# Kernel optimization log

Measured on AMD Instinct MI355X. Metric: run time of the kernel, lower is better.

The kernel has to match this reference:

```python
import jax, jax.numpy as jnp
import numpy as np

B, CH, T = 8, 512, 1024
HEADS = 8
KC = CH // HEADS  # 64
BLOCK = 256       # block_length


def setup_inputs() -> dict:
    key = jax.random.key(0)
    ks = jax.random.split(key, 10)
    s = 0.05
    x = jax.random.normal(ks[0], (B, CH, T), jnp.float32)
    c = jax.random.normal(ks[1], (B, CH, T), jnp.float32)
    attn_mask = jnp.ones((1, 1, T, T), jnp.int32)
    # 1x1 Conv1d weights are just [out, in] matrices over the channel dim.
    Wq = jax.random.normal(ks[2], (CH, CH), jnp.float32) * s
    bq = jax.random.normal(ks[3], (CH,), jnp.float32) * s
    Wk = jax.random.normal(ks[4], (CH, CH), jnp.float32) * s
    bk = jax.random.normal(ks[5], (CH,), jnp.float32) * s
    Wv = jax.random.normal(ks[6], (CH, CH), jnp.float32) * s
    bv = jax.random.normal(ks[7], (CH,), jnp.float32) * s
    Wo = jax.random.normal(ks[8], (CH, CH), jnp.float32) * s
    bo = jax.random.normal(ks[9], (CH,), jnp.float32) * s
    return {"x": x, "c": c, "attn_mask": attn_mask,
            "Wq": Wq, "bq": bq, "Wk": Wk, "bk": bk,
            "Wv": Wv, "bv": bv, "Wo": Wo, "bo": bo}


def _proj(W, b, z):
    # 1x1 Conv1d: [B,C,T] -> [B,O,T]
    return jnp.einsum('oc,bct->bot', W, z) + b[None, :, None]


def reference(x, c, attn_mask, Wq, bq, Wk, bk, Wv, bv, Wo, bo):
    q = _proj(Wq, bq, x)
    k = _proj(Wk, bk, c)
    v = _proj(Wv, bv, c)

    def split_heads(z):  # [B,C,T] -> [B,H,T,KC]
        return z.reshape(B, HEADS, KC, T).transpose(0, 1, 3, 2)

    qh, kh, vh = split_heads(q), split_heads(k), split_heads(v)

    scale = jnp.asarray(1.0 / np.sqrt(KC), qh.dtype)
    scores = jnp.einsum('bhtd,bhsd->bhts', qh * scale, kh)  # [B,H,T,T]

    r = jnp.arange(T)
    diff = jnp.abs(r[None, :] - r[:, None])  # |i - j|, [T,T]
    # proximal bias: -log(1 + |i-j|)
    scores = scores + (-jnp.log1p(diff.astype(scores.dtype)))[None, None]
    # attention mask: masked_fill(mask == 0, -1e4)
    scores = jnp.where(attn_mask == 0, jnp.asarray(-1e4, scores.dtype), scores)
    # block-length band mask: keep |i-j| <= BLOCK (triu(-BLOCK).tril(BLOCK))
    band = (diff <= BLOCK)[None, None]
    scores = jnp.where(band, scores, jnp.asarray(-1e4, scores.dtype))

    p_attn = jax.nn.softmax(scores, axis=-1)
    out = jnp.einsum('bhts,bhsd->bhtd', p_attn, vh)  # [B,H,T,KC]
    out = out.transpose(0, 1, 3, 2).reshape(B, CH, T)  # merge heads -> [B,C,T]
    return _proj(Wo, bo, out)
```

## Files before the change

kernel.cpp:

```cpp
#include <hip/hip_runtime.h>
#include <stdint.h>

typedef unsigned short u16;
typedef __attribute__((ext_vector_type(8))) __bf16 bf16x8;
typedef __attribute__((ext_vector_type(4))) float f32x4;

constexpr int B_ = 8, CH = 512, T = 1024, NH = 8, HD = 64, BAND = 256;

__device__ inline u16 f2b(float f) {
  union { float f; uint32_t u; } v; v.f = f;
  uint32_t r = (v.u + 0x7fffu + ((v.u >> 16) & 1u)) >> 16;
  return (u16)r;
}

__device__ inline f32x4 mfma16(bf16x8 a, bf16x8 b, f32x4 c) {
  return __builtin_amdgcn_mfma_f32_16x16x32_bf16(a, b, c, 0, 0, 0);
}

__device__ __forceinline__ void gld16(const void* g, void* l) {
  __builtin_amdgcn_global_load_lds((__attribute__((address_space(1))) void*)(g),
                                   (__attribute__((address_space(3))) void*)(l),
                                   16, 0, 0);
}

__device__ __forceinline__ float exp2_hw(float x) { return __builtin_amdgcn_exp2f(x); }

__global__ __launch_bounds__(256) void cvt_w(const float* __restrict__ wq, const float* __restrict__ wk,
                                             const float* __restrict__ wv, const float* __restrict__ wo,
                                             u16* __restrict__ out) {
  int idx = blockIdx.x * 256 + threadIdx.x;
  int w = idx >> 15;
  const float* src = (w == 0) ? wq : (w == 1) ? wk : (w == 2) ? wv : wo;
  int e = (idx & 32767) * 8;
  f32x4 a = *(const f32x4*)(src + e);
  f32x4 b = *(const f32x4*)(src + e + 4);
  union { u16 h[8]; bf16x8 v; } r;
  r.h[0] = f2b(a[0]); r.h[1] = f2b(a[1]); r.h[2] = f2b(a[2]); r.h[3] = f2b(a[3]);
  r.h[4] = f2b(b[0]); r.h[5] = f2b(b[1]); r.h[6] = f2b(b[2]); r.h[7] = f2b(b[3]);
  *(bf16x8*)(out + (w << 18) + e) = r.v;
}

__global__ __launch_bounds__(256) void tr_cvt(const float* __restrict__ x, const float* __restrict__ c,
                                              u16* __restrict__ xT, u16* __restrict__ cT) {
  __shared__ float tile[32][33];
  int z = blockIdx.z;
  const float* src = (z < B_) ? x : c;
  u16* dst = (z < B_) ? xT : cT;
  int b = (z < B_) ? z : z - B_;
  int t0 = blockIdx.x * 32, c0 = blockIdx.y * 32;
  int tx = threadIdx.x & 31, ty = threadIdx.x >> 5;
#pragma unroll
  for (int k = 0; k < 4; k++)
    tile[ty + 8 * k][tx] = src[(long)(b * CH + c0 + ty + 8 * k) * T + t0 + tx];
  __syncthreads();
#pragma unroll
  for (int k = 0; k < 4; k++)
    dst[(long)(b * T + t0 + ty + 8 * k) * CH + c0 + tx] = f2b(tile[tx][ty + 8 * k]);
}

template <int TN, typename OT>
__device__ __forceinline__ void gemm_core(const u16* __restrict__ Ab, int lda,
                                          const u16* __restrict__ Bb, int ldb,
                                          OT* __restrict__ Cb, int ldc,
                                          const float* __restrict__ bi, bool brow,
                                          int m0, int n0, int K, u16* smA, u16* smB) {
  int t = threadIdx.x, lane = t & 63, wave = t >> 6;
  int cl = lane & 15, quad = lane >> 4;
  int wm = wave >> 1, wn = wave & 1;
  int rr = t >> 3, gs = t & 7;
  constexpr int NW = TN / 32;
  f32x4 acc[4][NW] = {};
  auto stage = [&](int buf, int k0) {
#pragma unroll
    for (int j = 0; j < 4; j++) {
      int R = j * 32 + rr;
      int gc = (gs ^ (R & 7)) << 3;
      gld16(Ab + (long)(m0 + R) * lda + k0 + gc,
            (char*)(smA + buf * 128 * 64) + j * 4096 + wave * 1024);
      if (j < NW)
        gld16(Bb + (long)(n0 + R) * ldb + k0 + gc,
              (char*)(smB + buf * TN * 64) + j * 4096 + wave * 1024);
    }
  };
  stage(0, 0);
  int nk = K >> 6;
  for (int it = 0; it < nk; it++) {
    int cur = it & 1;
    __syncthreads();
    if (it + 1 < nk) stage(1 - cur, (it + 1) << 6);
    const u16* bA = smA + cur * 128 * 64;
    const u16* bB = smB + cur * TN * 64;
#pragma unroll
    for (int ks = 0; ks < 2; ks++) {
      int g2 = ((ks << 2) | quad) ^ (cl & 7);
      bf16x8 af[4], bb[NW];
#pragma unroll
      for (int i = 0; i < 4; i++)
        af[i] = *(const bf16x8*)&bA[(wm * 64 + i * 16 + cl) * 64 + g2 * 8];
#pragma unroll
      for (int i = 0; i < NW; i++)
        bb[i] = *(const bf16x8*)&bB[(wn * (TN / 2) + i * 16 + cl) * 64 + g2 * 8];
#pragma unroll
      for (int mi = 0; mi < 4; mi++)
#pragma unroll
        for (int ni = 0; ni < NW; ni++)
          acc[mi][ni] = mfma16(af[mi], bb[ni], acc[mi][ni]);
    }
  }
#pragma unroll
  for (int mi = 0; mi < 4; mi++) {
    int row = m0 + wm * 64 + mi * 16 + quad * 4;
#pragma unroll
    for (int ni = 0; ni < NW; ni++) {
      int col = n0 + wn * (TN / 2) + ni * 16 + cl;
#pragma unroll
      for (int r = 0; r < 4; r++) {
        float v = acc[mi][ni][r] + (brow ? bi[row + r] : bi[col]);
        if constexpr (sizeof(OT) == 2) Cb[(long)(row + r) * ldc + col] = f2b(v);
        else Cb[(long)(row + r) * ldc + col] = v;
      }
    }
  }
}

__global__ __launch_bounds__(256, 2) void gemm_qkv(const u16* __restrict__ xT, const u16* __restrict__ cT,
                                                   const u16* __restrict__ Wb,
                                                   u16* __restrict__ Qb, u16* __restrict__ Kb, u16* __restrict__ Vb,
                                                   const float* __restrict__ bq, const float* __restrict__ bk,
                                                   const float* __restrict__ bv) {
  __shared__ u16 smA[2 * 128 * 64], smB[2 * 128 * 64];
  const long TCH = (long)T * CH;
  int z = blockIdx.z, sec = z >> 3, zz = z & 7, bx = blockIdx.x;
  const u16 *Ab, *Bb; u16* Cb; const float* bi;
  int m0, n0, ldc; bool brow;
  if (sec == 0) {
    Ab = xT + zz * TCH; Bb = Wb;           Cb = Qb + zz * TCH;        bi = bq;
    m0 = (bx >> 2) * 128; n0 = (bx & 3) * 128; ldc = CH; brow = false;
  } else if (sec == 1) {
    Ab = cT + zz * TCH; Bb = Wb + 262144;  Cb = Kb + zz * TCH;        bi = bk;
    m0 = (bx >> 2) * 128; n0 = (bx & 3) * 128; ldc = CH; brow = false;
  } else {
    Ab = Wb + 2 * 262144; Bb = cT + zz * TCH; Cb = Vb + zz * (long)CH * T; bi = bv;
    m0 = (bx & 3) * 128; n0 = (bx >> 2) * 128; ldc = T; brow = true;
  }
  gemm_core<128, u16>(Ab, CH, Bb, CH, Cb, ldc, bi, brow, m0, n0, CH, smA, smB);
}

__global__ __launch_bounds__(256, 3) void gemm_o(const u16* __restrict__ Wo, const u16* __restrict__ AO,
                                                 float* __restrict__ out, const float* __restrict__ bo) {
  __shared__ u16 smA[2 * 128 * 64], smB[2 * 64 * 64];
  int z = blockIdx.z;
  gemm_core<64, float>(Wo, CH, AO + z * (long)T * CH, CH, out + z * (long)CH * T, T,
                       bo, true, blockIdx.y * 128, blockIdx.x * 64, CH, smA, smB);
}

__global__ __launch_bounds__(256, 3) void attn(const u16* __restrict__ Q, const u16* __restrict__ Kt,
                                               const u16* __restrict__ V, u16* __restrict__ AO) {
  __shared__ u16 sK[2][64 * 64];
  __shared__ u16 sV[2][64 * 64];
  __shared__ u16 sP[4][32 * 72];
  int lane = threadIdx.x & 63, wave = threadIdx.x >> 6;
  int cl = lane & 15, quad = lane >> 4;
  int bx = blockIdx.x;
  int xcd = bx & 7, ii = bx >> 3;
  int bh = xcd * 8 + (ii & 7);
  int qt = ii >> 3;
  int b = bh >> 3, h = bh & 7;
  int tq0 = qt * 128;
  int tqw = tq0 + wave * 16;
  const u16* qb0 = Q + ((long)(b * T + tqw + cl) * CH) + h * HD;
  const u16* qb1 = qb0 + (long)64 * CH;
  bf16x8 qf[2][2];
  qf[0][0] = *(const bf16x8*)(qb0 + quad * 8);
  qf[0][1] = *(const bf16x8*)(qb0 + 32 + quad * 8);
  qf[1][0] = *(const bf16x8*)(qb1 + quad * 8);
  qf[1][1] = *(const bf16x8*)(qb1 + 32 + quad * 8);
  f32x4 acc[2][4] = {};
  float lr[2][4] = {};
  float fir[2][4];
#pragma unroll
  for (int qg = 0; qg < 2; qg++)
#pragma unroll
    for (int r = 0; r < 4; r++) fir[qg][r] = (float)(tqw + qg * 64 + quad * 4 + r);
  int lo = tq0 - BAND; if (lo < 0) lo = 0;
  int hi = tq0 + 128 + BAND; if (hi > T) hi = T;
  int nt = (hi - lo) >> 6;

  int rl = lane >> 3, cg = lane & 7;
  const u16* ksrc = Kt + (long)b * T * CH + h * HD;
  const u16* vsrc = V + ((long)(b * CH + h * HD) * T);

#define STAGE(buf, j0)                                                          \
  {                                                                             \
    _Pragma("unroll")                                                           \
    for (int i = 0; i < 2; i++) {                                               \
      int r = wave * 16 + i * 8 + rl;                                           \
      int s = ((r >> 5) << 5) + ((r >> 4) & 1) + ((r & 15) << 1);               \
      gld16(ksrc + (long)(j0 + s) * CH + ((cg ^ (r & 7)) << 3),                 \
            (char*)&sK[buf][(wave * 16 + i * 8) * 64]);                         \
      gld16(vsrc + (long)r * T + (j0) + ((cg ^ (r & 7)) << 3),                  \
            (char*)&sV[buf][(wave * 16 + i * 8) * 64]);                         \
    }                                                                           \
  }

  STAGE(0, lo)
  constexpr float C2 = 0.125f * 1.4426950408889634f;
  for (int it = 0; it < nt; it++) {
    int cur = it & 1;
    int j0 = lo + it * 64;
    __syncthreads();
    if (it + 1 < nt) STAGE(1 - cur, j0 + 64)
    f32x4 sg[2][2][2];
#pragma unroll
    for (int p = 0; p < 2; p++)
#pragma unroll
      for (int sub = 0; sub < 2; sub++) {
        const u16* kr = &sK[cur][(p * 32 + sub * 16 + cl) * 64];
        bf16x8 k0 = *(const bf16x8*)&kr[((quad ^ (cl & 7)) << 3)];
        bf16x8 k1 = *(const bf16x8*)&kr[(((4 | quad) ^ (cl & 7)) << 3)];
        f32x4 z = {0.f, 0.f, 0.f, 0.f};
        sg[0][p][sub] = mfma16(qf[0][1], k1, mfma16(qf[0][0], k0, z));
        sg[1][p][sub] = mfma16(qf[1][1], k1, mfma16(qf[1][0], k0, z));
      }
#pragma unroll
    for (int qg = 0; qg < 2; qg++)
#pragma unroll
      for (int p = 0; p < 2; p++) {
        float jb = (float)(j0 + p * 32 + 2 * cl);
#pragma unroll
        for (int r = 0; r < 4; r++) {
          float de = fabsf(fir[qg][r] - jb);
          float dd = fabsf(fir[qg][r] - jb - 1.f);
          float pe = exp2_hw(sg[qg][p][0][r] * C2) * __builtin_amdgcn_rcpf(1.f + de);
          float po = exp2_hw(sg[qg][p][1][r] * C2) * __builtin_amdgcn_rcpf(1.f + dd);
          pe = (de <= 256.f) ? pe : 0.f;
          po = (dd <= 256.f) ? po : 0.f;
          lr[qg][r] += pe + po;
          uint32_t ue, uo;
          { union { float f; uint32_t u; } cv; cv.f = pe; ue = cv.u; cv.f = po; uo = cv.u; }
          uint32_t pk = ((uo + 0x8000u) & 0xffff0000u) | ((ue + 0x8000u) >> 16);
          *(uint32_t*)&sP[wave][(qg * 16 + quad * 4 + r) * 72 + p * 32 + 2 * cl] = pk;
        }
      }
#pragma unroll
    for (int ks = 0; ks < 2; ks++) {
      bf16x8 pf0 = *(bf16x8*)&sP[wave][cl * 72 + ks * 32 + quad * 8];
      bf16x8 pf1 = *(bf16x8*)&sP[wave][(16 + cl) * 72 + ks * 32 + quad * 8];
#pragma unroll
      for (int dg = 0; dg < 4; dg++) {
        bf16x8 vf = *(const bf16x8*)&sV[cur][(dg * 16 + cl) * 64 +
                                             ((((ks << 2) | quad) ^ (cl & 7)) << 3)];
        acc[0][dg] = mfma16(pf0, vf, acc[0][dg]);
        acc[1][dg] = mfma16(pf1, vf, acc[1][dg]);
      }
    }
  }
#undef STAGE
#pragma unroll
  for (int qg = 0; qg < 2; qg++) {
    float inv[4];
#pragma unroll
    for (int r = 0; r < 4; r++) {
      float s = lr[qg][r];
      s += __shfl_xor(s, 1); s += __shfl_xor(s, 2);
      s += __shfl_xor(s, 4); s += __shfl_xor(s, 8);
      inv[r] = __builtin_amdgcn_rcpf(s);
    }
#pragma unroll
    for (int dg = 0; dg < 4; dg++)
#pragma unroll
      for (int r = 0; r < 4; r++)
        AO[((long)(b * T + tqw + qg * 64 + quad * 4 + r) * CH) + h * HD + dg * 16 + cl] =
            f2b(acc[qg][dg][r] * inv[r]);
  }
}

extern "C" void kernel_launch(void* const* d_in, const int* in_sizes, int n_in,
                              void* d_out, int out_size, void* d_ws, size_t ws_size,
                              hipStream_t stream) {
  const float* x  = (const float*)d_in[0];
  const float* c  = (const float*)d_in[1];
  const float* Wq = (const float*)d_in[3];
  const float* bq = (const float*)d_in[4];
  const float* Wk = (const float*)d_in[5];
  const float* bk = (const float*)d_in[6];
  const float* Wv = (const float*)d_in[7];
  const float* bv = (const float*)d_in[8];
  const float* Wo = (const float*)d_in[9];
  const float* bo = (const float*)d_in[10];
  float* out = (float*)d_out;

  const long NT = (long)B_ * T * CH;
  u16* Wb = (u16*)d_ws;
  u16* xT = Wb + 4 * 262144;
  u16* cT = xT + NT;
  u16* Qb = cT + NT;
  u16* Kb = Qb + NT;
  u16* Vb = Kb + NT;
  u16* AO = xT;

  cvt_w<<<dim3(512), dim3(256), 0, stream>>>(Wq, Wk, Wv, Wo, Wb);
  tr_cvt<<<dim3(32, 16, 16), dim3(256), 0, stream>>>(x, c, xT, cT);
  gemm_qkv<<<dim3(32, 1, 24), dim3(256), 0, stream>>>(xT, cT, Wb, Qb, Kb, Vb, bq, bk, bv);
  attn<<<dim3(512), dim3(256), 0, stream>>>(Qb, Kb, Vb, AO);
  gemm_o<<<dim3(16, 4, 8), dim3(256), 0, stream>>>(Wb + 3 * 262144, AO, out, bo);
}
```

Baseline: 163.2 us.

## Merge weight conversion into transpose kernel and single-buffer GEMM LDS for occupancy

```diff
diff --git a/kernel.cpp b/kernel.cpp
--- a/kernel.cpp
+++ b/kernel.cpp
@@ -25,25 +25,26 @@
 
 __device__ __forceinline__ float exp2_hw(float x) { return __builtin_amdgcn_exp2f(x); }
 
-__global__ __launch_bounds__(256) void cvt_w(const float* __restrict__ wq, const float* __restrict__ wk,
-                                             const float* __restrict__ wv, const float* __restrict__ wo,
-                                             u16* __restrict__ out) {
-  int idx = blockIdx.x * 256 + threadIdx.x;
-  int w = idx >> 15;
-  const float* src = (w == 0) ? wq : (w == 1) ? wk : (w == 2) ? wv : wo;
-  int e = (idx & 32767) * 8;
-  f32x4 a = *(const f32x4*)(src + e);
-  f32x4 b = *(const f32x4*)(src + e + 4);
-  union { u16 h[8]; bf16x8 v; } r;
-  r.h[0] = f2b(a[0]); r.h[1] = f2b(a[1]); r.h[2] = f2b(a[2]); r.h[3] = f2b(a[3]);
-  r.h[4] = f2b(b[0]); r.h[5] = f2b(b[1]); r.h[6] = f2b(b[2]); r.h[7] = f2b(b[3]);
-  *(bf16x8*)(out + (w << 18) + e) = r.v;
-}
-
-__global__ __launch_bounds__(256) void tr_cvt(const float* __restrict__ x, const float* __restrict__ c,
-                                              u16* __restrict__ xT, u16* __restrict__ cT) {
+__global__ __launch_bounds__(256) void prep(const float* __restrict__ x, const float* __restrict__ c,
+                                            const float* __restrict__ wq, const float* __restrict__ wk,
+                                            const float* __restrict__ wv, const float* __restrict__ wo,
+                                            u16* __restrict__ xT, u16* __restrict__ cT,
+                                            u16* __restrict__ Wb) {
+  int z = blockIdx.z;
+  if (z == 16) {
+    int idx = (blockIdx.y * 32 + blockIdx.x) * 256 + threadIdx.x;
+    int w = idx >> 15;
+    const float* src = (w == 0) ? wq : (w == 1) ? wk : (w == 2) ? wv : wo;
+    int e = (idx & 32767) * 8;
+    f32x4 a = *(const f32x4*)(src + e);
+    f32x4 b = *(const f32x4*)(src + e + 4);
+    union { u16 h[8]; bf16x8 v; } r;
+    r.h[0] = f2b(a[0]); r.h[1] = f2b(a[1]); r.h[2] = f2b(a[2]); r.h[3] = f2b(a[3]);
+    r.h[4] = f2b(b[0]); r.h[5] = f2b(b[1]); r.h[6] = f2b(b[2]); r.h[7] = f2b(b[3]);
+    *(bf16x8*)(Wb + (w << 18) + e) = r.v;
+    return;
+  }
   __shared__ float tile[32][33];
-  int z = blockIdx.z;
   const float* src = (z < B_) ? x : c;
   u16* dst = (z < B_) ? xT : cT;
   int b = (z < B_) ? z : z - B_;
@@ -70,36 +71,27 @@
   int rr = t >> 3, gs = t & 7;
   constexpr int NW = TN / 32;
   f32x4 acc[4][NW] = {};
-  auto stage = [&](int buf, int k0) {
+  for (int k0 = 0; k0 < K; k0 += 64) {
+    __syncthreads();
 #pragma unroll
     for (int j = 0; j < 4; j++) {
       int R = j * 32 + rr;
       int gc = (gs ^ (R & 7)) << 3;
-      gld16(Ab + (long)(m0 + R) * lda + k0 + gc,
-            (char*)(smA + buf * 128 * 64) + j * 4096 + wave * 1024);
+      gld16(Ab + (long)(m0 + R) * lda + k0 + gc, (char*)smA + j * 4096 + wave * 1024);
       if (j < NW)
-        gld16(Bb + (long)(n0 + R) * ldb + k0 + gc,
-              (char*)(smB + buf * TN * 64) + j * 4096 + wave * 1024);
-    }
-  };
-  stage(0, 0);
-  int nk = K >> 6;
-  for (int it = 0; it < nk; it++) {
-    int cur = it & 1;
+        gld16(Bb + (long)(n0 + R) * ldb + k0 + gc, (char*)smB + j * 4096 + wave * 1024);
+    }
     __syncthreads();
-    if (it + 1 < nk) stage(1 - cur, (it + 1) << 6);
-    const u16* bA = smA + cur * 128 * 64;
-    const u16* bB = smB + cur * TN * 64;
 #pragma unroll
     for (int ks = 0; ks < 2; ks++) {
       int g2 = ((ks << 2) | quad) ^ (cl & 7);
       bf16x8 af[4], bb[NW];
 #pragma unroll
       for (int i = 0; i < 4; i++)
-        af[i] = *(const bf16x8*)&bA[(wm * 64 + i * 16 + cl) * 64 + g2 * 8];
+        af[i] = *(const bf16x8*)&smA[(wm * 64 + i * 16 + cl) * 64 + g2 * 8];
 #pragma unroll
       for (int i = 0; i < NW; i++)
-        bb[i] = *(const bf16x8*)&bB[(wn * (TN / 2) + i * 16 + cl) * 64 + g2 * 8];
+        bb[i] = *(const bf16x8*)&smB[(wn * (TN / 2) + i * 16 + cl) * 64 + g2 * 8];
 #pragma unroll
       for (int mi = 0; mi < 4; mi++)
 #pragma unroll
@@ -123,12 +115,12 @@
   }
 }
 
-__global__ __launch_bounds__(256, 2) void gemm_qkv(const u16* __restrict__ xT, const u16* __restrict__ cT,
+__global__ __launch_bounds__(256, 3) void gemm_qkv(const u16* __restrict__ xT, const u16* __restrict__ cT,
                                                    const u16* __restrict__ Wb,
                                                    u16* __restrict__ Qb, u16* __restrict__ Kb, u16* __restrict__ Vb,
                                                    const float* __restrict__ bq, const float* __restrict__ bk,
                                                    const float* __restrict__ bv) {
-  __shared__ u16 smA[2 * 128 * 64], smB[2 * 128 * 64];
+  __shared__ u16 smA[128 * 64], smB[128 * 64];
   const long TCH = (long)T * CH;
   int z = blockIdx.z, sec = z >> 3, zz = z & 7, bx = blockIdx.x;
   const u16 *Ab, *Bb; u16* Cb; const float* bi;
@@ -146,9 +138,9 @@
   gemm_core<128, u16>(Ab, CH, Bb, CH, Cb, ldc, bi, brow, m0, n0, CH, smA, smB);
 }
 
-__global__ __launch_bounds__(256, 3) void gemm_o(const u16* __restrict__ Wo, const u16* __restrict__ AO,
+__global__ __launch_bounds__(256, 4) void gemm_o(const u16* __restrict__ Wo, const u16* __restrict__ AO,
                                                  float* __restrict__ out, const float* __restrict__ bo) {
-  __shared__ u16 smA[2 * 128 * 64], smB[2 * 64 * 64];
+  __shared__ u16 smA[128 * 64], smB[64 * 64];
   int z = blockIdx.z;
   gemm_core<64, float>(Wo, CH, AO + z * (long)T * CH, CH, out + z * (long)CH * T, T,
                        bo, true, blockIdx.y * 128, blockIdx.x * 64, CH, smA, smB);
@@ -299,8 +291,7 @@
   u16* Vb = Kb + NT;
   u16* AO = xT;
 
-  cvt_w<<<dim3(512), dim3(256), 0, stream>>>(Wq, Wk, Wv, Wo, Wb);
-  tr_cvt<<<dim3(32, 16, 16), dim3(256), 0, stream>>>(x, c, xT, cT);
+  prep<<<dim3(32, 16, 17), dim3(256), 0, stream>>>(x, c, Wq, Wk, Wv, Wo, xT, cT, Wb);
   gemm_qkv<<<dim3(32, 1, 24), dim3(256), 0, stream>>>(xT, cT, Wb, Qb, Kb, Vb, bq, bk, bv);
   attn<<<dim3(512), dim3(256), 0, stream>>>(Qb, Kb, Vb, AO);
   gemm_o<<<dim3(16, 4, 8), dim3(256), 0, stream>>>(Wb + 3 * 262144, AO, out, bo);
```

After: 154.3 us. -5.5%, faster.
